# Kernel tuning notes

Hardware: AMD Instinct MI355X
Metric: run time of the kernel (lower is better)

Reference implementation:

```python
import jax, jax.numpy as jnp
import numpy as np
from jax import lax

B, PN, NS = 8, 16384, 256
KDIM, HID = 512, 384
HALF = HID // 2
EPS = 1e-5


def setup_inputs() -> dict:
    key = jax.random.key(0)
    ks = jax.random.split(key, 12)
    s = lambda fan: np.float32(1.0 / np.sqrt(fan))
    inp = {
        "p": jax.random.normal(ks[0], (B, PN, 3), jnp.float32),
        "N": NS,
        "patch_feature": jax.random.normal(ks[1], (B, KDIM, 1), jnp.float32),
        # Linear(k_dim, hidden)
        "W_feat": jax.random.normal(ks[2], (KDIM, HID), jnp.float32) * s(KDIM),
        "b_feat": jax.random.normal(ks[3], (HID,), jnp.float32) * s(KDIM),
        # Linear(3, hidden//2)
        "W_coord": jax.random.normal(ks[4], (3, HALF), jnp.float32) * s(3),
        "b_coord": jax.random.normal(ks[5], (HALF,), jnp.float32) * s(3),
        # Conv1d(hidden+hidden//2, hidden, 1) == per-point linear, weight (out,in)
        "W1": jax.random.normal(ks[6], (HID, HID + HALF), jnp.float32) * s(HID + HALF),
        "b1": jax.random.normal(ks[7], (HID,), jnp.float32) * s(HID + HALF),
        "g1": jnp.ones((HID,), jnp.float32),
        "be1": jnp.zeros((HID,), jnp.float32),
        # Conv1d(hidden, hidden, 1)
        "W2": jax.random.normal(ks[8], (HID, HID), jnp.float32) * s(HID),
        "b2": jax.random.normal(ks[9], (HID,), jnp.float32) * s(HID),
        "g2": jnp.ones((HID,), jnp.float32),
        "be2": jnp.zeros((HID,), jnp.float32),
    }
    return inp


def farthest_point_sample(points, k):
    """points: (B, N, C) -> (B, k, C). Deterministic start index 0 per batch."""
    b, n, c = points.shape

    def step(carry, _):
        dist, far = carry
        centroid = jnp.take_along_axis(points, far[:, None, None], axis=1)  # (B,1,C)
        d = jnp.sum((points - centroid) ** 2, axis=-1)                      # (B,N)
        dist = jnp.minimum(dist, d)
        new_far = jnp.argmax(dist, axis=-1)
        return (dist, new_far), far

    init = (jnp.full((b, n), 1e10, points.dtype), jnp.zeros((b,), jnp.int32))
    _, idx = lax.scan(step, init, None, length=k)  # idx: (k, B)
    idx = idx.T                                    # (B, k)
    return jnp.take_along_axis(points, idx[:, :, None], axis=1)  # (B,k,C)


def batchnorm(x, gamma, beta):
    """x: (B, L, C); training-mode BN over (B, L) per channel (biased var)."""
    mean = jnp.mean(x, axis=(0, 1))
    var = jnp.var(x, axis=(0, 1))
    return (x - mean) * lax.rsqrt(var + EPS) * gamma + beta


def reference(p, N, patch_feature, W_feat, b_feat, W_coord, b_coord,
              W1, b1, g1, be1, W2, b2, g2, be2):
    b, pn, _ = p.shape
    global_feat = patch_feature[..., 0] @ W_feat + b_feat          # (B, HID)
    global_feat = jnp.broadcast_to(global_feat[:, None, :], (b, N, HID))
    local_feat = p @ W_coord + b_coord                              # (B, PN, HALF)
    if N != pn:
        local_feat = farthest_point_sample(local_feat, N)           # (B, N, HALF)
    combined = jnp.concatenate([global_feat, local_feat], axis=-1)  # (B, N, HID+HALF)
    h = jnp.einsum("bnc,oc->bno", combined, W1) + b1
    h = jax.nn.relu(batchnorm(h, g1, be1))
    h = jnp.einsum("bnc,oc->bno", h, W2) + b2
    h = jax.nn.relu(batchnorm(h, g2, be2))
    return h  # (B, N, HID)
```

## Files before the change

### kernel.cpp

```cpp
#include <hip/hip_runtime.h>

#define BATCH 8
#define PN    16384
#define NSAMP 256
#define KDIM  512
#define HID   384
#define HALF  192
#define CIN   576
#define ROWS  2048
#define BN_EPS 1e-5f

#define OFF_GF   0
#define OFF_W1T  3072
#define OFF_W2T  224256
#define OFF_IDX  371712
#define OFF_H1   373760
#define OFF_H2   1160192
#define OFF_SUM1 1946624
#define OFF_SQ1  1947008
#define OFF_SUM2 1947392
#define OFF_SQ2  1947776

__global__ __launch_bounds__(1024) void k_main(const float* p, const float* Wc,
                                               const float* pf, const float* Wf,
                                               const float* bfe, const float* W1,
                                               const float* W2, float* ws) {
  __shared__ float s[KDIM];
  __shared__ float Msh[6];
  __shared__ unsigned long long red[2][16];
  int blk = blockIdx.x, t = threadIdx.x;

  if (blk >= 8) {
    if (blk < 16) {
      for (int sI = (blk - 8) * 1024 + t; sI < HID * CIN; sI += 8192) {
        int o = sI / CIN, c = sI % CIN;
        ws[OFF_W1T + c * HID + o] = W1[sI];
      }
    } else if (blk < 24) {
      for (int sI = (blk - 16) * 1024 + t; sI < HID * HID; sI += 8192) {
        int o = sI / HID, c = sI % HID;
        ws[OFF_W2T + c * HID + o] = W2[sI];
      }
    } else if (blk < 32) {
      int b = blk - 24;
      if (t < KDIM) s[t] = pf[b * KDIM + t];
      __syncthreads();
      if (t < HID) {
        float acc = bfe[t];
        for (int k = 0; k < KDIM; k++) acc = fmaf(s[k], Wf[k * HID + t], acc);
        ws[OFF_GF + b * HID + t] = acc;
      }
    } else {
      for (int i = t; i < 1536; i += 1024) ws[OFF_SUM1 + i] = 0.f;
    }
    return;
  }

  int b = blk;
  int* idx_out = (int*)(ws + OFF_IDX);

  if (t < 64) {
    double g0 = 0, g1 = 0, g2 = 0, g3 = 0, g4 = 0, g5 = 0;
    for (int k = t; k < HALF; k += 64) {
      double w0 = (double)Wc[k];
      double w1 = (double)Wc[HALF + k];
      double w2 = (double)Wc[2 * HALF + k];
      g0 += w0 * w0; g1 += w0 * w1; g2 += w0 * w2;
      g3 += w1 * w1; g4 += w1 * w2; g5 += w2 * w2;
    }
    for (int off = 32; off; off >>= 1) {
      g0 += __shfl_down(g0, off, 64); g1 += __shfl_down(g1, off, 64);
      g2 += __shfl_down(g2, off, 64); g3 += __shfl_down(g3, off, 64);
      g4 += __shfl_down(g4, off, 64); g5 += __shfl_down(g5, off, 64);
    }
    if (t == 0) {
      double l00 = sqrt(g0);
      double l10 = g1 / l00, l20 = g2 / l00;
      double l11 = sqrt(g3 - l10 * l10);
      double l21 = (g4 - l10 * l20) / l11;
      double l22 = sqrt(g5 - l20 * l20 - l21 * l21);
      Msh[0] = (float)l00; Msh[1] = (float)l10; Msh[2] = (float)l20;
      Msh[3] = (float)l11; Msh[4] = (float)l21; Msh[5] = (float)l22;
    }
  }
  __syncthreads();
  float m00 = Msh[0], m10 = Msh[1], m20 = Msh[2];
  float m11 = Msh[3], m21 = Msh[4], m22 = Msh[5];

  const float* pb = p + b * PN * 3;
  float qx[16], qy[16], qz[16], dist[16];
#pragma unroll
  for (int j = 0; j < 16; j++) {
    int i = (j << 10) + t;
    float x = pb[i * 3], y = pb[i * 3 + 1], z = pb[i * 3 + 2];
    qx[j] = fmaf(m00, x, fmaf(m10, y, m20 * z));
    qy[j] = fmaf(m11, y, m21 * z);
    qz[j] = m22 * z;
    dist[j] = 1e10f;
  }

  int far = 0, par = 0;
  for (int k = 0; k < NSAMP; k++) {
    if (t == 0) idx_out[b * NSAMP + k] = far;
    float x = pb[far * 3], y = pb[far * 3 + 1], z = pb[far * 3 + 2];
    float cx = fmaf(m00, x, fmaf(m10, y, m20 * z));
    float cy = fmaf(m11, y, m21 * z);
    float cz = m22 * z;
    float bv = -1.f; unsigned bj = 0;
#pragma unroll
    for (int j = 0; j < 16; j++) {
      float dx = qx[j] - cx, dy = qy[j] - cy, dz = qz[j] - cz;
      float d  = fmaf(dx, dx, fmaf(dy, dy, dz * dz));
      float nd = fminf(dist[j], d);
      dist[j] = nd;
      bool gt = nd > bv;
      bv = gt ? nd : bv;
      bj = gt ? (unsigned)j : bj;
    }
    unsigned bi = (bj << 10) + (unsigned)t;
    unsigned long long key =
        (((unsigned long long)__float_as_uint(bv)) << 32) | (unsigned)(~bi);
#pragma unroll
    for (int off = 32; off; off >>= 1) {
      unsigned long long o = __shfl_xor(key, off, 64);
      key = (o > key) ? o : key;
    }
    if ((t & 63) == 0) red[par][t >> 6] = key;
    __syncthreads();
    unsigned long long best = red[par][0];
#pragma unroll
    for (int w = 1; w < 16; w++) {
      unsigned long long o = red[par][w];
      best = (o > best) ? o : best;
    }
    far = (int)(~((unsigned)best));
    par ^= 1;
  }
}

__global__ __launch_bounds__(384) void k_gemm1(const float* p,
                                               const float* Wc,
                                               const float* bc,
                                               const float* b1,
                                               float* ws) {
  __shared__ __align__(16) float ct[CIN * 8];
  int t = threadIdx.x;
  int row0 = blockIdx.x * 8;
  const int* fidx = (const int*)(ws + OFF_IDX);
  for (int sI = t; sI < 8 * CIN; sI += 384) {
    int r = sI / CIN, c = sI % CIN;
    int row = row0 + r, b = row >> 8;
    float val;
    if (c < HID) {
      val = ws[OFF_GF + b * HID + c];
    } else {
      int co = c - HID;
      int i = fidx[row];
      const float* pp = p + (b * PN + i) * 3;
      val = bc[co];
      val = fmaf(pp[0], Wc[co], val);
      val = fmaf(pp[1], Wc[HALF + co], val);
      val = fmaf(pp[2], Wc[2 * HALF + co], val);
    }
    ct[c * 8 + r] = val;
  }
  __syncthreads();
  const float* w1t = ws + OFF_W1T;
  float acc[8] = {0.f, 0.f, 0.f, 0.f, 0.f, 0.f, 0.f, 0.f};
  for (int c = 0; c < CIN; c++) {
    float w = w1t[c * HID + t];
    float4 a0 = *(const float4*)(ct + c * 8);
    float4 a1 = *(const float4*)(ct + c * 8 + 4);
    acc[0] = fmaf(a0.x, w, acc[0]); acc[1] = fmaf(a0.y, w, acc[1]);
    acc[2] = fmaf(a0.z, w, acc[2]); acc[3] = fmaf(a0.w, w, acc[3]);
    acc[4] = fmaf(a1.x, w, acc[4]); acc[5] = fmaf(a1.y, w, acc[5]);
    acc[6] = fmaf(a1.z, w, acc[6]); acc[7] = fmaf(a1.w, w, acc[7]);
  }
  float bias = b1[t];
  float sv = 0.f, sq = 0.f;
#pragma unroll
  for (int r = 0; r < 8; r++) {
    float v = acc[r] + bias;
    ws[OFF_H1 + (row0 + r) * HID + t] = v;
    sv += v; sq = fmaf(v, v, sq);
  }
  atomicAdd(&ws[OFF_SUM1 + t], sv);
  atomicAdd(&ws[OFF_SQ1 + t], sq);
}

__global__ __launch_bounds__(384) void k_gemm2(const float* b2,
                                               const float* g1,
                                               const float* be1,
                                               float* ws) {
  __shared__ __align__(16) float ht[HID * 8];
  __shared__ float sc1s[HID], sh1s[HID];
  int t = threadIdx.x;
  int row0 = blockIdx.x * 8;
  {
    float m = ws[OFF_SUM1 + t] * (1.f / ROWS);
    float v = ws[OFF_SQ1 + t] * (1.f / ROWS) - m * m;
    float inv = 1.f / sqrtf(v + BN_EPS);
    float sc = inv * g1[t];
    sc1s[t] = sc;
    sh1s[t] = be1[t] - m * sc;
  }
  __syncthreads();
  for (int sI = t; sI < 8 * HID; sI += 384) {
    int r = sI / HID, c = sI % HID;
    float x = fmaf(ws[OFF_H1 + (row0 + r) * HID + c], sc1s[c], sh1s[c]);
    ht[c * 8 + r] = fmaxf(x, 0.f);
  }
  __syncthreads();
  const float* w2t = ws + OFF_W2T;
  float acc[8] = {0.f, 0.f, 0.f, 0.f, 0.f, 0.f, 0.f, 0.f};
  for (int c = 0; c < HID; c++) {
    float w = w2t[c * HID + t];
    float4 a0 = *(const float4*)(ht + c * 8);
    float4 a1 = *(const float4*)(ht + c * 8 + 4);
    acc[0] = fmaf(a0.x, w, acc[0]); acc[1] = fmaf(a0.y, w, acc[1]);
    acc[2] = fmaf(a0.z, w, acc[2]); acc[3] = fmaf(a0.w, w, acc[3]);
    acc[4] = fmaf(a1.x, w, acc[4]); acc[5] = fmaf(a1.y, w, acc[5]);
    acc[6] = fmaf(a1.z, w, acc[6]); acc[7] = fmaf(a1.w, w, acc[7]);
  }
  float bias = b2[t];
  float sv = 0.f, sq = 0.f;
#pragma unroll
  for (int r = 0; r < 8; r++) {
    float v = acc[r] + bias;
    ws[OFF_H2 + (row0 + r) * HID + t] = v;
    sv += v; sq = fmaf(v, v, sq);
  }
  atomicAdd(&ws[OFF_SUM2 + t], sv);
  atomicAdd(&ws[OFF_SQ2 + t], sq);
}

__global__ __launch_bounds__(256) void k_out(const float* ws, const float* g2,
                                             const float* be2, float* out) {
  int gid = blockIdx.x * 256 + threadIdx.x;
  int i = gid * 4;
  int c = i % HID;
  float4 h  = *(const float4*)(ws + OFF_H2 + i);
  float4 s2 = *(const float4*)(ws + OFF_SUM2 + c);
  float4 q2 = *(const float4*)(ws + OFF_SQ2 + c);
  float4 gv = *(const float4*)(g2 + c);
  float4 bv = *(const float4*)(be2 + c);
  float4 r;
#define BN2(comp) {                                                  \
    float m  = s2.comp * (1.f / ROWS);                               \
    float v  = q2.comp * (1.f / ROWS) - m * m;                       \
    float sc = (1.f / sqrtf(v + BN_EPS)) * gv.comp;                  \
    float sh = bv.comp - m * sc;                                     \
    r.comp = fmaxf(fmaf(h.comp, sc, sh), 0.f); }
  BN2(x) BN2(y) BN2(z) BN2(w)
#undef BN2
  ((float4*)out)[gid] = r;
}

extern "C" void kernel_launch(void* const* d_in, const int* in_sizes, int n_in,
                              void* d_out, int out_size, void* d_ws, size_t ws_size,
                              hipStream_t stream) {
  const float* p   = (const float*)d_in[0];
  const float* pf  = (const float*)d_in[2];
  const float* Wf  = (const float*)d_in[3];
  const float* bfe = (const float*)d_in[4];
  const float* Wc  = (const float*)d_in[5];
  const float* bc  = (const float*)d_in[6];
  const float* W1  = (const float*)d_in[7];
  const float* b1  = (const float*)d_in[8];
  const float* g1  = (const float*)d_in[9];
  const float* be1 = (const float*)d_in[10];
  const float* W2  = (const float*)d_in[11];
  const float* b2  = (const float*)d_in[12];
  const float* g2  = (const float*)d_in[13];
  const float* be2 = (const float*)d_in[14];
  float* ws = (float*)d_ws;

  hipLaunchKernelGGL(k_main,  dim3(33),  dim3(1024), 0, stream,
                     p, Wc, pf, Wf, bfe, W1, W2, ws);
  hipLaunchKernelGGL(k_gemm1, dim3(256), dim3(384), 0, stream, p, Wc, bc, b1, ws);
  hipLaunchKernelGGL(k_gemm2, dim3(256), dim3(384), 0, stream, b2, g1, be1, ws);
  hipLaunchKernelGGL(k_out,   dim3(768), dim3(256), 0, stream,
                     ws, g2, be2, (float*)d_out);
}
```

Measured before the change: 599.1 us.

## Vectorize FPS distance update and split argmax into max-then-index reduction

The farthest-point-sampling loop now stores the per-thread point coordinates and distances as float2 vectors, so the distance update can use packed FMA/min. The 64-bit key argmax reduction is replaced by a float max reduction over shuffles and LDS. Threads holding the global max then resolve the lowest index through a shared atomicMin. This removes 64-bit shuffle and compare work on the serial critical path, at the cost of a second __syncthreads per iteration plus an atomic.

After: 524.6 us. 1.14x faster.

```diff
diff --git a/kernel.cpp b/kernel.cpp
--- a/kernel.cpp
+++ b/kernel.cpp
@@ -21,13 +21,16 @@
 #define OFF_SUM2 1947392
 #define OFF_SQ2  1947776
 
+typedef float v2f __attribute__((ext_vector_type(2)));
+
 __global__ __launch_bounds__(1024) void k_main(const float* p, const float* Wc,
                                                const float* pf, const float* Wf,
                                                const float* bfe, const float* W1,
                                                const float* W2, float* ws) {
   __shared__ float s[KDIM];
   __shared__ float Msh[6];
-  __shared__ unsigned long long red[2][16];
+  __shared__ __align__(16) float redv[2][16];
+  __shared__ int widx[2];
   int blk = blockIdx.x, t = threadIdx.x;
 
   if (blk >= 8) {
@@ -88,52 +91,76 @@
   float m11 = Msh[3], m21 = Msh[4], m22 = Msh[5];
 
   const float* pb = p + b * PN * 3;
-  float qx[16], qy[16], qz[16], dist[16];
-#pragma unroll
-  for (int j = 0; j < 16; j++) {
-    int i = (j << 10) + t;
-    float x = pb[i * 3], y = pb[i * 3 + 1], z = pb[i * 3 + 2];
-    qx[j] = fmaf(m00, x, fmaf(m10, y, m20 * z));
-    qy[j] = fmaf(m11, y, m21 * z);
-    qz[j] = m22 * z;
-    dist[j] = 1e10f;
+  v2f qx[8], qy[8], qz[8], dist[8];
+#pragma unroll
+  for (int j = 0; j < 8; j++) {
+    int i0 = ((2 * j) << 10) + t;
+    int i1 = i0 + 1024;
+    float x0 = pb[i0 * 3], y0 = pb[i0 * 3 + 1], z0 = pb[i0 * 3 + 2];
+    float x1 = pb[i1 * 3], y1 = pb[i1 * 3 + 1], z1 = pb[i1 * 3 + 2];
+    qx[j] = (v2f){fmaf(m00, x0, fmaf(m10, y0, m20 * z0)),
+                  fmaf(m00, x1, fmaf(m10, y1, m20 * z1))};
+    qy[j] = (v2f){fmaf(m11, y0, m21 * z0), fmaf(m11, y1, m21 * z1)};
+    qz[j] = (v2f){m22 * z0, m22 * z1};
+    dist[j] = (v2f){1e10f, 1e10f};
   }
 
   int far = 0, par = 0;
   for (int k = 0; k < NSAMP; k++) {
-    if (t == 0) idx_out[b * NSAMP + k] = far;
+    if (t == 0) {
+      idx_out[b * NSAMP + k] = far;
+      widx[par] = 0x7fffffff;
+    }
     float x = pb[far * 3], y = pb[far * 3 + 1], z = pb[far * 3 + 2];
     float cx = fmaf(m00, x, fmaf(m10, y, m20 * z));
     float cy = fmaf(m11, y, m21 * z);
     float cz = m22 * z;
-    float bv = -1.f; unsigned bj = 0;
-#pragma unroll
-    for (int j = 0; j < 16; j++) {
-      float dx = qx[j] - cx, dy = qy[j] - cy, dz = qz[j] - cz;
-      float d  = fmaf(dx, dx, fmaf(dy, dy, dz * dz));
-      float nd = fminf(dist[j], d);
-      dist[j] = nd;
-      bool gt = nd > bv;
-      bv = gt ? nd : bv;
-      bj = gt ? (unsigned)j : bj;
-    }
-    unsigned bi = (bj << 10) + (unsigned)t;
-    unsigned long long key =
-        (((unsigned long long)__float_as_uint(bv)) << 32) | (unsigned)(~bi);
-#pragma unroll
-    for (int off = 32; off; off >>= 1) {
-      unsigned long long o = __shfl_xor(key, off, 64);
-      key = (o > key) ? o : key;
-    }
-    if ((t & 63) == 0) red[par][t >> 6] = key;
+    v2f cxv = (v2f){cx, cx}, cyv = (v2f){cy, cy}, czv = (v2f){cz, cz};
+#pragma unroll
+    for (int j = 0; j < 8; j++) {
+      v2f dx = qx[j] - cxv, dy = qy[j] - cyv, dz = qz[j] - czv;
+      v2f d = __builtin_elementwise_fma(
+          dx, dx, __builtin_elementwise_fma(dy, dy, dz * dz));
+      dist[j] = __builtin_elementwise_min(dist[j], d);
+    }
+    float a0 = fmaxf(dist[0].x, dist[0].y);
+    float a1 = fmaxf(dist[1].x, dist[1].y);
+    float a2 = fmaxf(dist[2].x, dist[2].y);
+    float a3 = fmaxf(dist[3].x, dist[3].y);
+    float a4 = fmaxf(dist[4].x, dist[4].y);
+    float a5 = fmaxf(dist[5].x, dist[5].y);
+    float a6 = fmaxf(dist[6].x, dist[6].y);
+    float a7 = fmaxf(dist[7].x, dist[7].y);
+    float b0 = fmaxf(fmaxf(a0, a1), a2);
+    float b1 = fmaxf(fmaxf(a3, a4), a5);
+    float tmax = fmaxf(fmaxf(b0, b1), fmaxf(a6, a7));
+    float m = tmax;
+#pragma unroll
+    for (int off = 32; off; off >>= 1) m = fmaxf(m, __shfl_xor(m, off, 64));
+    if ((t & 63) == 0) redv[par][t >> 6] = m;
     __syncthreads();
-    unsigned long long best = red[par][0];
-#pragma unroll
-    for (int w = 1; w < 16; w++) {
-      unsigned long long o = red[par][w];
-      best = (o > best) ? o : best;
-    }
-    far = (int)(~((unsigned)best));
+    float4 r0 = *(const float4*)&redv[par][0];
+    float4 r1 = *(const float4*)&redv[par][4];
+    float4 r2 = *(const float4*)&redv[par][8];
+    float4 r3 = *(const float4*)&redv[par][12];
+    float g01 = fmaxf(fmaxf(r0.x, r0.y), r0.z);
+    float g02 = fmaxf(fmaxf(r0.w, r1.x), r1.y);
+    float g03 = fmaxf(fmaxf(r1.z, r1.w), r2.x);
+    float g04 = fmaxf(fmaxf(r2.y, r2.z), r2.w);
+    float g05 = fmaxf(fmaxf(r3.x, r3.y), r3.z);
+    float gmax = fmaxf(fmaxf(fmaxf(g01, g02), g03),
+                       fmaxf(fmaxf(g04, g05), r3.w));
+    if (tmax == gmax) {
+      int mi = 0x7fffffff;
+#pragma unroll
+      for (int j = 0; j < 8; j++) {
+        if (dist[j].x == gmax) mi = min(mi, ((2 * j) << 10) + t);
+        if (dist[j].y == gmax) mi = min(mi, ((2 * j + 1) << 10) + t);
+      }
+      atomicMin(&widx[par], mi);
+    }
+    __syncthreads();
+    far = widx[par];
     par ^= 1;
   }
 }
```
